# Performance work log

Measured on AMD Instinct MI355X. Metric: run time of the kernel, lower is better.

## Reference

```python
import jax, jax.numpy as jnp
import numpy as np

B, T, C, H = 2, 2048, 1024, 16
D = C // H  # head dim, even
NEG = -1e10  # masked_fill value used by the torch module (not -inf)


def _rope_cache(dim, max_positions):
    # Faithful to source: theta_i = 1/10000**(-2*(i-1)/dim), i = arange(dim//2)
    i = jnp.arange(dim // 2, dtype=jnp.float32)
    theta = 1.0 / (10000.0 ** (-2.0 * (i - 1.0) / dim))
    ang = jnp.arange(max_positions, dtype=jnp.float32)[:, None] * theta[None, :]  # [T, D/2]
    return jnp.cos(ang), jnp.sin(ang)


def _apply_rope(x, cos, sin):
    # x: [B,H,T,D]; consecutive pairs form complex numbers (x[...,2j], x[...,2j+1])
    xp = x.reshape(*x.shape[:-1], D // 2, 2)
    xr, xi = xp[..., 0], xp[..., 1]
    rr = xr * cos - xi * sin
    ri = xr * sin + xi * cos
    return jnp.stack([rr, ri], axis=-1).reshape(x.shape)


def setup_inputs() -> dict:
    key = jax.random.key(0)
    ks = jax.random.split(key, 5)
    s = 1.0 / np.sqrt(C)
    return {
        'x': jax.random.normal(ks[0], (B, T, C), jnp.float32),
        'Wq': jax.random.normal(ks[1], (C, C), jnp.float32) * s,
        'bq': jnp.zeros((C,), jnp.float32),
        'Wk': jax.random.normal(ks[2], (C, C), jnp.float32) * s,
        'bk': jnp.zeros((C,), jnp.float32),
        'Wv': jax.random.normal(ks[3], (C, C), jnp.float32) * s,
        'bv': jnp.zeros((C,), jnp.float32),
        'Wp': jax.random.normal(ks[4], (C, C), jnp.float32) * s,
        'bp': jnp.zeros((C,), jnp.float32),
    }


def reference(x, Wq, bq, Wk, bk, Wv, bv, Wp, bp):
    cos, sin = _rope_cache(D, T)  # [T, D/2]
    def split_heads(h):
        return h.reshape(B, T, H, D).transpose(0, 2, 1, 3)  # [B,H,T,D]
    q = split_heads(x @ Wq.T + bq)
    k = split_heads(x @ Wk.T + bk)
    v = split_heads(x @ Wv.T + bv)
    q = _apply_rope(q, cos, sin)
    k = _apply_rope(k, cos, sin)
    att = jnp.einsum('bhqd,bhkd->bhqk', q, k) * (1.0 / np.sqrt(D))  # [B,H,T,T]
    causal = jnp.tril(jnp.ones((T, T), bool))
    att = jnp.where(causal, att, NEG)
    att = jax.nn.softmax(att, axis=-1)
    y = jnp.einsum('bhqk,bhkd->bhqd', att, v)
    y = y.transpose(0, 2, 1, 3).reshape(B, T, C)
    return y @ Wp.T + bp
```

## Files before the change

kernel.cpp:

```cpp
#include <hip/hip_runtime.h>

#define SEQ 2048
#define CDIM 1024
#define NHEAD 16
#define HDIM 64
#define NSLOT 40

typedef __bf16 bf16x8 __attribute__((ext_vector_type(8)));
typedef __bf16 bf16x4v __attribute__((ext_vector_type(4)));
typedef float f32x4 __attribute__((ext_vector_type(4)));

typedef const __attribute__((address_space(1))) char* gcp_t;
typedef __attribute__((address_space(3))) char* lcp_t;

__device__ __forceinline__ void gload16(const void* g, void* l) {
    __builtin_amdgcn_global_load_lds((gcp_t)g, (lcp_t)l, 16, 0, 0);
}

__device__ __forceinline__ unsigned short f2bf(float f) {
    unsigned int u = __float_as_uint(f);
    u += 0x7fffu + ((u >> 16) & 1u);
    return (unsigned short)(u >> 16);
}

__device__ __forceinline__ float bflo(unsigned int u) { return __uint_as_float(u << 16); }
__device__ __forceinline__ float bfhi(unsigned int u) { return __uint_as_float(u & 0xffff0000u); }

__device__ __forceinline__ int swz16(int r) { return ((r >> 1) & 3) << 4; }


__global__ void cvt_kernel(const float* __restrict__ src, unsigned short* __restrict__ dst, int n4) {
    int i = blockIdx.x * blockDim.x + threadIdx.x;
    if (i < n4) {
        float4 v = ((const float4*)src)[i];
        ushort4 o;
        o.x = f2bf(v.x); o.y = f2bf(v.y); o.z = f2bf(v.z); o.w = f2bf(v.w);
        ((ushort4*)dst)[i] = o;
    }
}

__global__ void cvtw_kernel(const float* __restrict__ Wq, const float* __restrict__ Wk,
                            const float* __restrict__ Wv, const float* __restrict__ Wp,
                            unsigned short* __restrict__ wqkv, unsigned short* __restrict__ wpb) {
    int i = blockIdx.x * blockDim.x + threadIdx.x;
    int which = i >> 18, r = i & 262143;
    const float* s = (which == 0) ? Wq : (which == 1) ? Wk : (which == 2) ? Wv : Wp;
    unsigned short* d = (which < 3) ? (wqkv + (size_t)which * 1048576) : wpb;
    float4 v = ((const float4*)s)[r];
    ushort4 o;
    o.x = f2bf(v.x); o.y = f2bf(v.y); o.z = f2bf(v.z); o.w = f2bf(v.w);
    ((ushort4*)d)[r] = o;
}

__global__ void rope_kernel(float2* __restrict__ cstab) {
    int idx = blockIdx.x * blockDim.x + threadIdx.x;
    int j = idx & 31, t = idx >> 5;
    float e = -2.0f * ((float)j - 1.0f) / 64.0f;
    float denom = (float)pow(10000.0, (double)e);
    float theta = 1.0f / denom;
    float ang = (float)t * theta;
    cstab[idx] = make_float2(cosf(ang), sinf(ang));
}

template <int MODE, int BM>
__global__ __launch_bounds__(256) void gemm_bt(
    const unsigned short* __restrict__ A, const unsigned short* __restrict__ Bm,
    const float* __restrict__ b0, const float* __restrict__ b1, const float* __restrict__ b2,
    unsigned short* __restrict__ qb, unsigned short* __restrict__ kb,
    unsigned short* __restrict__ vtb, float* __restrict__ outf,
    const float2* __restrict__ cstab)
{
    constexpr int K = 1024;
    constexpr int NIT = K / 32;
    constexpr int NR = (BM == 128) ? 4 : 2;
    __shared__ __align__(16) char As[2][BM * 64];
    __shared__ __align__(16) char Bs[2][128 * 64];
    const int tid = threadIdx.x, lane = tid & 63, wid = tid >> 6;
    const int m0 = blockIdx.y * BM, n0 = blockIdx.x * 128;
    const int wr = (BM == 128) ? ((wid >> 1) * 64) : 0;
    const int wc = (BM == 128) ? ((wid & 1) * 64) : (wid * 32);

    f32x4 acc[4][NR] = {};

    const char* Ag = (const char*)(A + (size_t)m0 * K);
    const char* Bg = (const char*)(Bm + (size_t)n0 * K);
    const int r0 = tid >> 2, cb = (tid & 3) * 16;
    const int ldsw = wid << 10;

    auto stage = [&](int k0, int bufi) {
        char* Ad = As[bufi];
        char* Bd = Bs[bufi];
        gload16(Ag + (size_t)r0 * 2048 + k0 * 2 + (cb ^ swz16(r0)), Ad + ldsw);
        if constexpr (BM == 128)
            gload16(Ag + (size_t)(r0 + 64) * 2048 + k0 * 2 + (cb ^ swz16(r0 + 64)), Ad + 4096 + ldsw);
        gload16(Bg + (size_t)r0 * 2048 + k0 * 2 + (cb ^ swz16(r0)), Bd + ldsw);
        gload16(Bg + (size_t)(r0 + 64) * 2048 + k0 * 2 + (cb ^ swz16(r0 + 64)), Bd + 4096 + ldsw);
    };

    stage(0, 0);
    __syncthreads();

    for (int it = 0; it < NIT; ++it) {
        const int cur = it & 1;
        if (it + 1 < NIT) stage((it + 1) * 32, cur ^ 1);
        const char* Ac = As[cur];
        const char* Bc = Bs[cur];
        const int fs = (lane >> 4) * 16;
        bf16x8 af[4], bfr[NR];
#pragma unroll
        for (int am = 0; am < 4; ++am) {
            const int r = wr + am * 16 + (lane & 15);
            af[am] = *(const bf16x8*)(Ac + r * 64 + (fs ^ swz16(r)));
        }
#pragma unroll
        for (int an = 0; an < NR; ++an) {
            const int r = wc + an * 16 + (lane & 15);
            bfr[an] = *(const bf16x8*)(Bc + r * 64 + (fs ^ swz16(r)));
        }
#pragma unroll
        for (int am = 0; am < 4; ++am)
#pragma unroll
            for (int an = 0; an < NR; ++an)
                acc[am][an] = __builtin_amdgcn_mfma_f32_16x16x32_bf16(af[am], bfr[an], acc[am][an], 0, 0, 0);
        __syncthreads();
    }

    if (MODE == 0) {
        const float QSCL = 0.18033688011112042f;
#pragma unroll
        for (int an = 0; an < NR; ++an) {
            const int ng = n0 + wc + an * 16 + (lane & 15);
            const int which = ng >> 10, nl = ng & 1023;
            const int h = nl >> 6, d = nl & 63;
            const float* bptr = (which == 0) ? b0 : (which == 1) ? b1 : b2;
            const float bias = bptr[nl];
            if (which < 2) {
                unsigned short* dst = (which == 0) ? qb : kb;
                const float qs = (which == 0) ? QSCL : 1.0f;
                const int j = d >> 1;
#pragma unroll
                for (int am = 0; am < 4; ++am) {
#pragma unroll
                    for (int i = 0; i < 4; ++i) {
                        const int row = m0 + wr + am * 16 + (lane >> 4) * 4 + i;
                        const int bb = row >> 11, t = row & 2047;
                        float v = acc[am][an][i] + bias;
                        float p = __shfl_xor(v, 1);
                        const float2 cs = cstab[t * 32 + j];
                        v = (d & 1) ? fmaf(v, cs.x, p * cs.y) : fmaf(v, cs.x, -p * cs.y);
                        dst[((size_t)((bb * 16 + h) * 2048 + t)) * 64 + d] = f2bf(v * qs);
                    }
                }
            } else {
#pragma unroll
                for (int am = 0; am < 4; ++am) {
                    const int rowb = m0 + wr + am * 16 + (lane >> 4) * 4;
                    const int bb = rowb >> 11, t = rowb & 2047;
                    ushort4 pk;
                    pk.x = f2bf(acc[am][an][0] + bias);
                    pk.y = f2bf(acc[am][an][1] + bias);
                    pk.z = f2bf(acc[am][an][2] + bias);
                    pk.w = f2bf(acc[am][an][3] + bias);
                    *(ushort4*)(vtb + ((size_t)((bb * 16 + h) * 64 + d)) * 2048 + t) = pk;
                }
            }
        }
    } else {
#pragma unroll
        for (int an = 0; an < NR; ++an) {
            const int col = n0 + wc + an * 16 + (lane & 15);
            const float bias = b0[col];
#pragma unroll
            for (int am = 0; am < 4; ++am)
#pragma unroll
                for (int i = 0; i < 4; ++i) {
                    const int row = m0 + wr + am * 16 + (lane >> 4) * 4 + i;
                    outf[(size_t)row * 1024 + col] = acc[am][an][i] + bias;
                }
        }
    }
}

__global__ __launch_bounds__(256) void attn_kernel(
    const unsigned short* __restrict__ qb, const unsigned short* __restrict__ kb,
    const unsigned short* __restrict__ vtb, unsigned short* __restrict__ pb,
    float2* __restrict__ ml)
{
    __shared__ __align__(16) unsigned short Ks[2][64 * 64];
    __shared__ __align__(16) unsigned short Vs[2][64 * 64];
    __shared__ __align__(16) unsigned short Ps[4][32 * 64];
    const int tid = threadIdx.x, lane = tid & 63, wid = tid >> 6;
    const int bh = blockIdx.x;
    const int y = blockIdx.y;
    int qt, ck, nc;
    if (y < 16)      { qt = 15 - (y >> 2); ck = y & 3; nc = 4; }
    else if (y < 28) { int t2 = y - 16; int k3 = t2 / 3; qt = 11 - k3; ck = t2 - k3 * 3; nc = 3; }
    else if (y < 36) { int t2 = y - 28; qt = 7 - (t2 >> 1); ck = t2 & 1; nc = 2; }
    else             { qt = 3 - (y - 36); ck = 0; nc = 1; }
    const int nt = 2 * qt + 2;
    const int t0 = ck * nt / nc, t1 = (ck + 1) * nt / nc;
    const int q0 = qt * 128;
    const int qw = q0 + wid * 32;
    const unsigned short* Qg = qb + (size_t)bh * SEQ * HDIM;
    const char* Kg = (const char*)(kb + (size_t)bh * SEQ * HDIM);
    const char* Vg = (const char*)(vtb + (size_t)bh * HDIM * SEQ);

    bf16x8 qf[2][2];
#pragma unroll
    for (int am = 0; am < 2; ++am)
#pragma unroll
        for (int kf = 0; kf < 2; ++kf)
            qf[am][kf] = *(const bf16x8*)(Qg + (size_t)(qw + am * 16 + (lane & 15)) * 64 + kf * 32 + (lane >> 4) * 8);

    f32x4 o[4][2] = {};
    float mrun[2] = {-3e38f, -3e38f};
    float lrun[2] = {0.0f, 0.0f};

    const int cr0 = tid >> 3, cc0 = ((tid & 7) * 16) ^ ((cr0 & 7) << 4);
    const int cr1 = cr0 + 32, cc1 = ((tid & 7) * 16) ^ ((cr1 & 7) << 4);
    const int ldsw = wid << 10;

    auto stage = [&](int kt, int bufi) {
        const size_t kv0 = (size_t)kt * 64;
        gload16(Kg + (kv0 + cr0) * 128 + cc0, (char*)Ks[bufi] + ldsw);
        gload16(Kg + (kv0 + cr1) * 128 + cc1, (char*)Ks[bufi] + 4096 + ldsw);
        gload16(Vg + (size_t)cr0 * 4096 + kv0 * 2 + cc0, (char*)Vs[bufi] + ldsw);
        gload16(Vg + (size_t)cr1 * 4096 + kv0 * 2 + cc1, (char*)Vs[bufi] + 4096 + ldsw);
    };

    stage(t0, 0);
    __syncthreads();

    for (int kt = t0; kt < t1; ++kt) {
        const int cur = (kt - t0) & 1;
        if (kt + 1 < t1) stage(kt + 1, cur ^ 1);
        const int kv0 = kt * 64;
        if (kv0 <= qw + 31) {
            f32x4 s[4][2] = {};
            __builtin_amdgcn_s_setprio(1);
#pragma unroll
            for (int kf = 0; kf < 2; ++kf) {
                bf16x8 kfr[4];
#pragma unroll
                for (int an = 0; an < 4; ++an) {
                    const int r = an * 16 + (lane & 15);
                    kfr[an] = *(const bf16x8*)((const char*)Ks[cur] + r * 128 + ((kf * 64 + (lane >> 4) * 16) ^ ((r & 7) << 4)));
                }
#pragma unroll
                for (int an = 0; an < 4; ++an)
#pragma unroll
                    for (int am = 0; am < 2; ++am)
                        s[an][am] = __builtin_amdgcn_mfma_f32_16x16x32_bf16(kfr[an], qf[am][kf], s[an][am], 0, 0, 0);
            }
            __builtin_amdgcn_s_setprio(0);
            const bool need_mask = (kv0 + 63 > qw);
#pragma unroll
            for (int am = 0; am < 2; ++am) {
                const int qg = qw + am * 16 + (lane & 15);
                const int kbase = kv0 + ((lane >> 4) << 2);
                float p[4][4];
                float mx = -3e38f;
#pragma unroll
                for (int an = 0; an < 4; ++an)
#pragma unroll
                    for (int i = 0; i < 4; ++i) {
                        float v = s[an][am][i];
                        if (need_mask && (kbase + an * 16 + i > qg)) v = -3e38f;
                        p[an][i] = v;
                        mx = fmaxf(mx, v);
                    }
                mx = fmaxf(mx, __shfl_xor(mx, 16));
                mx = fmaxf(mx, __shfl_xor(mx, 32));
                if (!__all(mx <= mrun[am] + 8.0f)) {
                    const float mnew = fmaxf(mrun[am], mx);
                    const float fsc = __builtin_amdgcn_exp2f(mrun[am] - mnew);
                    lrun[am] *= fsc;
#pragma unroll
                    for (int dn = 0; dn < 4; ++dn) o[dn][am] *= fsc;
                    mrun[am] = mnew;
                }
                float rs = 0.0f;
#pragma unroll
                for (int an = 0; an < 4; ++an)
#pragma unroll
                    for (int i = 0; i < 4; ++i) {
                        p[an][i] = __builtin_amdgcn_exp2f(p[an][i] - mrun[am]);
                        rs += p[an][i];
                    }
                rs += __shfl_xor(rs, 16);
                rs += __shfl_xor(rs, 32);
                lrun[am] += rs;
                const int ql = am * 16 + (lane & 15);
                char* pbs = (char*)Ps[wid] + ql * 128;
                const int xr = (ql & 7) << 4;
                const int gb = (lane >> 4) << 3;
#pragma unroll
                for (int an = 0; an < 4; ++an) {
                    bf16x4v pk;
                    pk[0] = (__bf16)p[an][0]; pk[1] = (__bf16)p[an][1];
                    pk[2] = (__bf16)p[an][2]; pk[3] = (__bf16)p[an][3];
                    *(bf16x4v*)(pbs + ((an * 32 + gb) ^ xr)) = pk;
                }
            }
            __builtin_amdgcn_s_setprio(1);
#pragma unroll
            for (int kf = 0; kf < 2; ++kf) {
                bf16x8 vf[4], pf[2];
#pragma unroll
                for (int dn = 0; dn < 4; ++dn) {
                    const int r = dn * 16 + (lane & 15);
                    vf[dn] = *(const bf16x8*)((const char*)Vs[cur] + r * 128 + ((kf * 64 + (lane >> 4) * 16) ^ ((r & 7) << 4)));
                }
#pragma unroll
                for (int am = 0; am < 2; ++am) {
                    const int ql = am * 16 + (lane & 15);
                    pf[am] = *(const bf16x8*)((const char*)Ps[wid] + ql * 128 + ((kf * 64 + (lane >> 4) * 16) ^ ((ql & 7) << 4)));
                }
#pragma unroll
                for (int dn = 0; dn < 4; ++dn)
#pragma unroll
                    for (int am = 0; am < 2; ++am)
                        o[dn][am] = __builtin_amdgcn_mfma_f32_16x16x32_bf16(vf[dn], pf[am], o[dn][am], 0, 0, 0);
            }
            __builtin_amdgcn_s_setprio(0);
        }
        __syncthreads();
    }

    {
        const size_t sbase = (size_t)bh * NSLOT + y;
#pragma unroll
        for (int am = 0; am < 2; ++am) {
            const int qloc = wid * 32 + am * 16 + (lane & 15);
            unsigned short* prow = pb + (sbase * 128 + qloc) * 64;
#pragma unroll
            for (int dn = 0; dn < 4; ++dn) {
                const int d = dn * 16 + ((lane >> 4) << 2);
                bf16x4v pk;
                pk[0] = (__bf16)o[dn][am][0];
                pk[1] = (__bf16)o[dn][am][1];
                pk[2] = (__bf16)o[dn][am][2];
                pk[3] = (__bf16)o[dn][am][3];
                *(bf16x4v*)(prow + d) = pk;
            }
            if ((lane >> 4) == 0) ml[sbase * 128 + qloc] = make_float2(mrun[am], lrun[am]);
        }
    }
}

__global__ __launch_bounds__(256) void combine_kernel(
    const unsigned short* __restrict__ pb, const float2* __restrict__ ml,
    unsigned short* __restrict__ yb)
{
    const int bx = blockIdx.x, bh = blockIdx.y;
    const int qt = bx >> 1, qh = (bx & 1) * 64;
    const int b = bh >> 4, h = bh & 15;
    int base, nc;
    if (qt >= 12)      { base = (15 - qt) * 4;      nc = 4; }
    else if (qt >= 8)  { base = 16 + (11 - qt) * 3; nc = 3; }
    else if (qt >= 4)  { base = 28 + (7 - qt) * 2;  nc = 2; }
    else               { base = 36 + (3 - qt);      nc = 1; }
    const int t = threadIdx.x;
    const int q = qh + (t >> 2);
    const int d0 = (t & 3) * 16;
    const size_t sbase = (size_t)bh * NSLOT + base;

    float m[4], l[4];
    float M = -3e38f;
#pragma unroll
    for (int c = 0; c < 4; ++c)
        if (c < nc) {
            float2 v = ml[(sbase + c) * 128 + q];
            m[c] = v.x; l[c] = v.y;
            M = fmaxf(M, v.x);
        }
    float L = 0.0f;
    float w[4];
#pragma unroll
    for (int c = 0; c < 4; ++c)
        if (c < nc) {
            w[c] = __builtin_amdgcn_exp2f(m[c] - M);
            L += l[c] * w[c];
        }
    const float invL = 1.0f / L;

    float acc[16] = {};
#pragma unroll
    for (int c = 0; c < 4; ++c)
        if (c < nc) {
            const float wc = w[c] * invL;
            const uint4* src = (const uint4*)(pb + ((sbase + c) * 128 + q) * 64 + d0);
            uint4 A = src[0], B = src[1];
            const unsigned int ua[8] = {A.x, A.y, A.z, A.w, B.x, B.y, B.z, B.w};
#pragma unroll
            for (int k = 0; k < 8; ++k) {
                acc[2 * k]     = fmaf(wc, bflo(ua[k]), acc[2 * k]);
                acc[2 * k + 1] = fmaf(wc, bfhi(ua[k]), acc[2 * k + 1]);
            }
        }

    unsigned int outw[8];
#pragma unroll
    for (int k = 0; k < 8; ++k)
        outw[k] = (unsigned int)f2bf(acc[2 * k]) | ((unsigned int)f2bf(acc[2 * k + 1]) << 16);
    uint4* dst = (uint4*)(yb + (size_t)(b * SEQ + qt * 128 + q) * CDIM + h * 64 + d0);
    dst[0] = make_uint4(outw[0], outw[1], outw[2], outw[3]);
    dst[1] = make_uint4(outw[4], outw[5], outw[6], outw[7]);
}


extern "C" void kernel_launch(void* const* d_in, const int* in_sizes, int n_in,
                              void* d_out, int out_size, void* d_ws, size_t ws_size,
                              hipStream_t stream) {
    (void)in_sizes; (void)n_in; (void)out_size; (void)ws_size;
    const float* x  = (const float*)d_in[0];
    const float* Wq = (const float*)d_in[1];
    const float* bq = (const float*)d_in[2];
    const float* Wk = (const float*)d_in[3];
    const float* bk = (const float*)d_in[4];
    const float* Wv = (const float*)d_in[5];
    const float* bv = (const float*)d_in[6];
    const float* Wp = (const float*)d_in[7];
    const float* bp = (const float*)d_in[8];
    float* out = (float*)d_out;

    char* ws = (char*)d_ws;
    size_t off = 0;
    auto take = [&](size_t bytes) -> char* {
        char* p = ws + off;
        off = (off + bytes + 255) & ~(size_t)255;
        return p;
    };
    float2* cstab = (float2*)take((size_t)SEQ * 32 * 8);
    unsigned short* xb   = (unsigned short*)take((size_t)4096 * 1024 * 2);
    unsigned short* wqkv = (unsigned short*)take((size_t)3 * 1024 * 1024 * 2);
    unsigned short* wpb  = (unsigned short*)take((size_t)1024 * 1024 * 2);
    unsigned short* qbuf = (unsigned short*)take((size_t)32 * SEQ * HDIM * 2);
    unsigned short* kbuf = (unsigned short*)take((size_t)32 * SEQ * HDIM * 2);
    unsigned short* vtb  = (unsigned short*)take((size_t)32 * HDIM * SEQ * 2);
    unsigned short* yb   = (unsigned short*)take((size_t)4096 * 1024 * 2);
    unsigned short* pbuf = (unsigned short*)take((size_t)32 * NSLOT * 128 * 64 * 2);
    float2* mlb          = (float2*)take((size_t)32 * NSLOT * 128 * 8);

    rope_kernel<<<256, 256, 0, stream>>>(cstab);
    cvt_kernel<<<4096, 256, 0, stream>>>(x, xb, 1048576);
    cvtw_kernel<<<4096, 256, 0, stream>>>(Wq, Wk, Wv, Wp, wqkv, wpb);

    dim3 g0(24, 32);
    gemm_bt<0, 128><<<g0, 256, 0, stream>>>(xb, wqkv, bq, bk, bv, qbuf, kbuf, vtb, nullptr, cstab);
    dim3 g1(32, NSLOT);
    attn_kernel<<<g1, 256, 0, stream>>>(qbuf, kbuf, vtb, pbuf, mlb);
    dim3 gc(32, 32);
    combine_kernel<<<gc, 256, 0, stream>>>(pbuf, mlb, yb);
    dim3 g2(8, 64);
    gemm_bt<1, 64><<<g2, 256, 0, stream>>>(yb, wpb, bp, nullptr, nullptr, nullptr, nullptr, nullptr, out, cstab);
}
```

Measured before the change: 142.3 us.

## Replace split-KV attention plus combine with single-pass per-wave register-loaded attention

Removes the split-KV partitioning and the separate combine kernel. Each block now handles one full 128-row query tile, and each wave walks only its own causal range. K and V fragments are loaded straight from global memory into registers, with K prefetched one tile ahead, in place of the shared-memory double-buffered staging and block barriers. Query tiles are paired heavy/light and blocks are remapped across XCDs for load balance, and launch bounds request 2 blocks per CU. This drops the partial-result round trip and one kernel launch, but each wave now re-reads K/V from global or L2 without block-level sharing and gives up split-KV parallelism for long rows.

```diff
diff --git a/kernel.cpp b/kernel.cpp
--- a/kernel.cpp
+++ b/kernel.cpp
@@ -4,7 +4,6 @@
 #define CDIM 1024
 #define NHEAD 16
 #define HDIM 64
-#define NSLOT 40
 
 typedef __bf16 bf16x8 __attribute__((ext_vector_type(8)));
 typedef __bf16 bf16x4v __attribute__((ext_vector_type(4)));
@@ -22,9 +21,6 @@
     u += 0x7fffu + ((u >> 16) & 1u);
     return (unsigned short)(u >> 16);
 }
-
-__device__ __forceinline__ float bflo(unsigned int u) { return __uint_as_float(u << 16); }
-__device__ __forceinline__ float bfhi(unsigned int u) { return __uint_as_float(u & 0xffff0000u); }
 
 __device__ __forceinline__ int swz16(int r) { return ((r >> 1) & 3) << 4; }
 
@@ -181,29 +177,25 @@
     }
 }
 
-__global__ __launch_bounds__(256) void attn_kernel(
+__global__ __launch_bounds__(256, 2) void attn_kernel(
     const unsigned short* __restrict__ qb, const unsigned short* __restrict__ kb,
-    const unsigned short* __restrict__ vtb, unsigned short* __restrict__ pb,
-    float2* __restrict__ ml)
+    const unsigned short* __restrict__ vtb, unsigned short* __restrict__ yb)
 {
-    __shared__ __align__(16) unsigned short Ks[2][64 * 64];
-    __shared__ __align__(16) unsigned short Vs[2][64 * 64];
     __shared__ __align__(16) unsigned short Ps[4][32 * 64];
     const int tid = threadIdx.x, lane = tid & 63, wid = tid >> 6;
-    const int bh = blockIdx.x;
-    const int y = blockIdx.y;
-    int qt, ck, nc;
-    if (y < 16)      { qt = 15 - (y >> 2); ck = y & 3; nc = 4; }
-    else if (y < 28) { int t2 = y - 16; int k3 = t2 / 3; qt = 11 - k3; ck = t2 - k3 * 3; nc = 3; }
-    else if (y < 36) { int t2 = y - 28; qt = 7 - (t2 >> 1); ck = t2 & 1; nc = 2; }
-    else             { qt = 3 - (y - 36); ck = 0; nc = 1; }
-    const int nt = 2 * qt + 2;
-    const int t0 = ck * nt / nc, t1 = (ck + 1) * nt / nc;
-    const int q0 = qt * 128;
-    const int qw = q0 + wid * 32;
+    const int bid = blockIdx.x;
+    const int wg = (bid & 7) * 64 + (bid >> 3);
+    const int bh = wg >> 4;
+    const int xx = wg & 15;
+    const int qt = (xx & 1) ? (15 - (xx >> 1)) : (xx >> 1);
+    const int b = bh >> 4, h = bh & 15;
+    const int qw = qt * 128 + wid * 32;
+
     const unsigned short* Qg = qb + (size_t)bh * SEQ * HDIM;
     const char* Kg = (const char*)(kb + (size_t)bh * SEQ * HDIM);
     const char* Vg = (const char*)(vtb + (size_t)bh * HDIM * SEQ);
+    const char* Kbase = Kg + (lane & 15) * 128 + (lane >> 4) * 16;
+    const char* Vbase = Vg + (lane & 15) * 4096 + (lane >> 4) * 16;
 
     bf16x8 qf[2][2];
 #pragma unroll
@@ -215,197 +207,130 @@
     f32x4 o[4][2] = {};
     float mrun[2] = {-3e38f, -3e38f};
     float lrun[2] = {0.0f, 0.0f};
-
-    const int cr0 = tid >> 3, cc0 = ((tid & 7) * 16) ^ ((cr0 & 7) << 4);
-    const int cr1 = cr0 + 32, cc1 = ((tid & 7) * 16) ^ ((cr1 & 7) << 4);
-    const int ldsw = wid << 10;
-
-    auto stage = [&](int kt, int bufi) {
-        const size_t kv0 = (size_t)kt * 64;
-        gload16(Kg + (kv0 + cr0) * 128 + cc0, (char*)Ks[bufi] + ldsw);
-        gload16(Kg + (kv0 + cr1) * 128 + cc1, (char*)Ks[bufi] + 4096 + ldsw);
-        gload16(Vg + (size_t)cr0 * 4096 + kv0 * 2 + cc0, (char*)Vs[bufi] + ldsw);
-        gload16(Vg + (size_t)cr1 * 4096 + kv0 * 2 + cc1, (char*)Vs[bufi] + 4096 + ldsw);
-    };
-
-    stage(t0, 0);
-    __syncthreads();
-
-    for (int kt = t0; kt < t1; ++kt) {
-        const int cur = (kt - t0) & 1;
-        if (kt + 1 < t1) stage(kt + 1, cur ^ 1);
+    const int nt = (qw >> 6) + 1;
+
+    bf16x8 ka[4][2], kn[4][2], vf[4][2];
+#pragma unroll
+    for (int an = 0; an < 4; ++an)
+#pragma unroll
+        for (int kf = 0; kf < 2; ++kf)
+            ka[an][kf] = *(const bf16x8*)(Kbase + an * 2048 + kf * 64);
+
+    for (int kt = 0; kt < nt; ++kt) {
         const int kv0 = kt * 64;
-        if (kv0 <= qw + 31) {
-            f32x4 s[4][2] = {};
-            __builtin_amdgcn_s_setprio(1);
-#pragma unroll
-            for (int kf = 0; kf < 2; ++kf) {
-                bf16x8 kfr[4];
-#pragma unroll
-                for (int an = 0; an < 4; ++an) {
-                    const int r = an * 16 + (lane & 15);
-                    kfr[an] = *(const bf16x8*)((const char*)Ks[cur] + r * 128 + ((kf * 64 + (lane >> 4) * 16) ^ ((r & 7) << 4)));
-                }
-#pragma unroll
-                for (int an = 0; an < 4; ++an)
-#pragma unroll
-                    for (int am = 0; am < 2; ++am)
-                        s[an][am] = __builtin_amdgcn_mfma_f32_16x16x32_bf16(kfr[an], qf[am][kf], s[an][am], 0, 0, 0);
+#pragma unroll
+        for (int dn = 0; dn < 4; ++dn)
+#pragma unroll
+            for (int kf = 0; kf < 2; ++kf)
+                vf[dn][kf] = *(const bf16x8*)(Vbase + dn * 65536 + kv0 * 2 + kf * 64);
+        f32x4 s[4][2] = {};
+        __builtin_amdgcn_s_setprio(1);
+#pragma unroll
+        for (int kf = 0; kf < 2; ++kf)
+#pragma unroll
+            for (int an = 0; an < 4; ++an)
+#pragma unroll
+                for (int am = 0; am < 2; ++am)
+                    s[an][am] = __builtin_amdgcn_mfma_f32_16x16x32_bf16(ka[an][kf], qf[am][kf], s[an][am], 0, 0, 0);
+        __builtin_amdgcn_s_setprio(0);
+        if (kt + 1 < nt) {
+            const char* Kt = Kbase + (size_t)(kv0 + 64) * 128;
+#pragma unroll
+            for (int an = 0; an < 4; ++an)
+#pragma unroll
+                for (int kf = 0; kf < 2; ++kf)
+                    kn[an][kf] = *(const bf16x8*)(Kt + an * 2048 + kf * 64);
+        }
+        const bool need_mask = (kv0 + 63 > qw);
+#pragma unroll
+        for (int am = 0; am < 2; ++am) {
+            const int qg = qw + am * 16 + (lane & 15);
+            const int kbase = kv0 + ((lane >> 4) << 2);
+            float p[4][4];
+            float mx = -3e38f;
+#pragma unroll
+            for (int an = 0; an < 4; ++an)
+#pragma unroll
+                for (int i = 0; i < 4; ++i) {
+                    float v = s[an][am][i];
+                    if (need_mask && (kbase + an * 16 + i > qg)) v = -3e38f;
+                    p[an][i] = v;
+                    mx = fmaxf(mx, v);
+                }
+            mx = fmaxf(mx, __shfl_xor(mx, 16));
+            mx = fmaxf(mx, __shfl_xor(mx, 32));
+            if (!__all(mx <= mrun[am] + 8.0f)) {
+                const float mnew = fmaxf(mrun[am], mx);
+                const float fsc = __builtin_amdgcn_exp2f(mrun[am] - mnew);
+                lrun[am] *= fsc;
+#pragma unroll
+                for (int dn = 0; dn < 4; ++dn) o[dn][am] *= fsc;
+                mrun[am] = mnew;
             }
-            __builtin_amdgcn_s_setprio(0);
-            const bool need_mask = (kv0 + 63 > qw);
+            float rs = 0.0f;
+#pragma unroll
+            for (int an = 0; an < 4; ++an)
+#pragma unroll
+                for (int i = 0; i < 4; ++i) {
+                    p[an][i] = __builtin_amdgcn_exp2f(p[an][i] - mrun[am]);
+                    rs += p[an][i];
+                }
+            rs += __shfl_xor(rs, 16);
+            rs += __shfl_xor(rs, 32);
+            lrun[am] += rs;
+            const int ql = am * 16 + (lane & 15);
+            char* pbs = (char*)Ps[wid] + ql * 128;
+            const int xr = (ql & 7) << 4;
+            const int gb = (lane >> 4) << 3;
+#pragma unroll
+            for (int an = 0; an < 4; ++an) {
+                bf16x4v pk;
+                pk[0] = (__bf16)p[an][0]; pk[1] = (__bf16)p[an][1];
+                pk[2] = (__bf16)p[an][2]; pk[3] = (__bf16)p[an][3];
+                *(bf16x4v*)(pbs + ((an * 32 + gb) ^ xr)) = pk;
+            }
+        }
+        __builtin_amdgcn_s_setprio(1);
+#pragma unroll
+        for (int kf = 0; kf < 2; ++kf) {
+            bf16x8 pf[2];
 #pragma unroll
             for (int am = 0; am < 2; ++am) {
-                const int qg = qw + am * 16 + (lane & 15);
-                const int kbase = kv0 + ((lane >> 4) << 2);
-                float p[4][4];
-                float mx = -3e38f;
-#pragma unroll
-                for (int an = 0; an < 4; ++an)
-#pragma unroll
-                    for (int i = 0; i < 4; ++i) {
-                        float v = s[an][am][i];
-                        if (need_mask && (kbase + an * 16 + i > qg)) v = -3e38f;
-                        p[an][i] = v;
-                        mx = fmaxf(mx, v);
-                    }
-                mx = fmaxf(mx, __shfl_xor(mx, 16));
-                mx = fmaxf(mx, __shfl_xor(mx, 32));
-                if (!__all(mx <= mrun[am] + 8.0f)) {
-                    const float mnew = fmaxf(mrun[am], mx);
-                    const float fsc = __builtin_amdgcn_exp2f(mrun[am] - mnew);
-                    lrun[am] *= fsc;
-#pragma unroll
-                    for (int dn = 0; dn < 4; ++dn) o[dn][am] *= fsc;
-                    mrun[am] = mnew;
-                }
-                float rs = 0.0f;
-#pragma unroll
-                for (int an = 0; an < 4; ++an)
-#pragma unroll
-                    for (int i = 0; i < 4; ++i) {
-                        p[an][i] = __builtin_amdgcn_exp2f(p[an][i] - mrun[am]);
-                        rs += p[an][i];
-                    }
-                rs += __shfl_xor(rs, 16);
-                rs += __shfl_xor(rs, 32);
-                lrun[am] += rs;
                 const int ql = am * 16 + (lane & 15);
-                char* pbs = (char*)Ps[wid] + ql * 128;
-                const int xr = (ql & 7) << 4;
-                const int gb = (lane >> 4) << 3;
-#pragma unroll
-                for (int an = 0; an < 4; ++an) {
-                    bf16x4v pk;
-                    pk[0] = (__bf16)p[an][0]; pk[1] = (__bf16)p[an][1];
-                    pk[2] = (__bf16)p[an][2]; pk[3] = (__bf16)p[an][3];
-                    *(bf16x4v*)(pbs + ((an * 32 + gb) ^ xr)) = pk;
-                }
+                pf[am] = *(const bf16x8*)((const char*)Ps[wid] + ql * 128 + ((kf * 64 + (lane >> 4) * 16) ^ ((ql & 7) << 4)));
             }
-            __builtin_amdgcn_s_setprio(1);
-#pragma unroll
-            for (int kf = 0; kf < 2; ++kf) {
-                bf16x8 vf[4], pf[2];
-#pragma unroll
-                for (int dn = 0; dn < 4; ++dn) {
-                    const int r = dn * 16 + (lane & 15);
-                    vf[dn] = *(const bf16x8*)((const char*)Vs[cur] + r * 128 + ((kf * 64 + (lane >> 4) * 16) ^ ((r & 7) << 4)));
-                }
-#pragma unroll
-                for (int am = 0; am < 2; ++am) {
-                    const int ql = am * 16 + (lane & 15);
-                    pf[am] = *(const bf16x8*)((const char*)Ps[wid] + ql * 128 + ((kf * 64 + (lane >> 4) * 16) ^ ((ql & 7) << 4)));
-                }
-#pragma unroll
-                for (int dn = 0; dn < 4; ++dn)
-#pragma unroll
-                    for (int am = 0; am < 2; ++am)
-                        o[dn][am] = __builtin_amdgcn_mfma_f32_16x16x32_bf16(vf[dn], pf[am], o[dn][am], 0, 0, 0);
-            }
-            __builtin_amdgcn_s_setprio(0);
-        }
-        __syncthreads();
-    }
-
-    {
-        const size_t sbase = (size_t)bh * NSLOT + y;
-#pragma unroll
-        for (int am = 0; am < 2; ++am) {
-            const int qloc = wid * 32 + am * 16 + (lane & 15);
-            unsigned short* prow = pb + (sbase * 128 + qloc) * 64;
-#pragma unroll
-            for (int dn = 0; dn < 4; ++dn) {
-                const int d = dn * 16 + ((lane >> 4) << 2);
-                bf16x4v pk;
-                pk[0] = (__bf16)o[dn][am][0];
-                pk[1] = (__bf16)o[dn][am][1];
-                pk[2] = (__bf16)o[dn][am][2];
-                pk[3] = (__bf16)o[dn][am][3];
-                *(bf16x4v*)(prow + d) = pk;
-            }
-            if ((lane >> 4) == 0) ml[sbase * 128 + qloc] = make_float2(mrun[am], lrun[am]);
-        }
-    }
-}
-
-__global__ __launch_bounds__(256) void combine_kernel(
-    const unsigned short* __restrict__ pb, const float2* __restrict__ ml,
-    unsigned short* __restrict__ yb)
-{
-    const int bx = blockIdx.x, bh = blockIdx.y;
-    const int qt = bx >> 1, qh = (bx & 1) * 64;
-    const int b = bh >> 4, h = bh & 15;
-    int base, nc;
-    if (qt >= 12)      { base = (15 - qt) * 4;      nc = 4; }
-    else if (qt >= 8)  { base = 16 + (11 - qt) * 3; nc = 3; }
-    else if (qt >= 4)  { base = 28 + (7 - qt) * 2;  nc = 2; }
-    else               { base = 36 + (3 - qt);      nc = 1; }
-    const int t = threadIdx.x;
-    const int q = qh + (t >> 2);
-    const int d0 = (t & 3) * 16;
-    const size_t sbase = (size_t)bh * NSLOT + base;
-
-    float m[4], l[4];
-    float M = -3e38f;
-#pragma unroll
-    for (int c = 0; c < 4; ++c)
-        if (c < nc) {
-            float2 v = ml[(sbase + c) * 128 + q];
-            m[c] = v.x; l[c] = v.y;
-            M = fmaxf(M, v.x);
-        }
-    float L = 0.0f;
-    float w[4];
-#pragma unroll
-    for (int c = 0; c < 4; ++c)
-        if (c < nc) {
-            w[c] = __builtin_amdgcn_exp2f(m[c] - M);
-            L += l[c] * w[c];
-        }
-    const float invL = 1.0f / L;
-
-    float acc[16] = {};
-#pragma unroll
-    for (int c = 0; c < 4; ++c)
-        if (c < nc) {
-            const float wc = w[c] * invL;
-            const uint4* src = (const uint4*)(pb + ((sbase + c) * 128 + q) * 64 + d0);
-            uint4 A = src[0], B = src[1];
-            const unsigned int ua[8] = {A.x, A.y, A.z, A.w, B.x, B.y, B.z, B.w};
-#pragma unroll
-            for (int k = 0; k < 8; ++k) {
-                acc[2 * k]     = fmaf(wc, bflo(ua[k]), acc[2 * k]);
-                acc[2 * k + 1] = fmaf(wc, bfhi(ua[k]), acc[2 * k + 1]);
-            }
-        }
-
-    unsigned int outw[8];
-#pragma unroll
-    for (int k = 0; k < 8; ++k)
-        outw[k] = (unsigned int)f2bf(acc[2 * k]) | ((unsigned int)f2bf(acc[2 * k + 1]) << 16);
-    uint4* dst = (uint4*)(yb + (size_t)(b * SEQ + qt * 128 + q) * CDIM + h * 64 + d0);
-    dst[0] = make_uint4(outw[0], outw[1], outw[2], outw[3]);
-    dst[1] = make_uint4(outw[4], outw[5], outw[6], outw[7]);
+#pragma unroll
+            for (int dn = 0; dn < 4; ++dn)
+#pragma unroll
+                for (int am = 0; am < 2; ++am)
+                    o[dn][am] = __builtin_amdgcn_mfma_f32_16x16x32_bf16(vf[dn][kf], pf[am], o[dn][am], 0, 0, 0);
+        }
+        __builtin_amdgcn_s_setprio(0);
+        if (kt + 1 < nt) {
+#pragma unroll
+            for (int an = 0; an < 4; ++an)
+#pragma unroll
+                for (int kf = 0; kf < 2; ++kf)
+                    ka[an][kf] = kn[an][kf];
+        }
+    }
+
+#pragma unroll
+    for (int am = 0; am < 2; ++am) {
+        const float inv = 1.0f / lrun[am];
+        const int qg = qw + am * 16 + (lane & 15);
+        unsigned short* yrow = yb + (size_t)(b * SEQ + qg) * CDIM + h * 64;
+#pragma unroll
+        for (int dn = 0; dn < 4; ++dn) {
+            const int d = dn * 16 + ((lane >> 4) << 2);
+            bf16x4v pk;
+            pk[0] = (__bf16)(o[dn][am][0] * inv);
+            pk[1] = (__bf16)(o[dn][am][1] * inv);
+            pk[2] = (__bf16)(o[dn][am][2] * inv);
+            pk[3] = (__bf16)(o[dn][am][3] * inv);
+            *(bf16x4v*)(yrow + d) = pk;
+        }
+    }
 }
 
 
@@ -439,8 +364,6 @@
     unsigned short* kbuf = (unsigned short*)take((size_t)32 * SEQ * HDIM * 2);
     unsigned short* vtb  = (unsigned short*)take((size_t)32 * HDIM * SEQ * 2);
     unsigned short* yb   = (unsigned short*)take((size_t)4096 * 1024 * 2);
-    unsigned short* pbuf = (unsigned short*)take((size_t)32 * NSLOT * 128 * 64 * 2);
-    float2* mlb          = (float2*)take((size_t)32 * NSLOT * 128 * 8);
 
     rope_kernel<<<256, 256, 0, stream>>>(cstab);
     cvt_kernel<<<4096, 256, 0, stream>>>(x, xb, 1048576);
@@ -448,10 +371,7 @@
 
     dim3 g0(24, 32);
     gemm_bt<0, 128><<<g0, 256, 0, stream>>>(xb, wqkv, bq, bk, bv, qbuf, kbuf, vtb, nullptr, cstab);
-    dim3 g1(32, NSLOT);
-    attn_kernel<<<g1, 256, 0, stream>>>(qbuf, kbuf, vtb, pbuf, mlb);
-    dim3 gc(32, 32);
-    combine_kernel<<<gc, 256, 0, stream>>>(pbuf, mlb, yb);
+    attn_kernel<<<512, 256, 0, stream>>>(qbuf, kbuf, vtb, yb);
     dim3 g2(8, 64);
     gemm_bt<1, 64><<<g2, 256, 0, stream>>>(yb, wpb, bp, nullptr, nullptr, nullptr, nullptr, nullptr, out, cstab);
 }
```

New measurement: 197.6 us. 1.39x slower.
